# Kernel tuning notes

Measured on AMD Instinct MI355X. Metric: run time of the kernel, lower is better.

## Reference

```python
import jax, jax.numpy as jnp
import numpy as np

B, S, EMBED_DIM, FFN_DIM, N_QUBITS = 8, 4096, 768, 3072, 8

# Quantum math: each qubit starts in |0>, gets RX(x_i) then RY(theta_i), then <Z_i>.
# Since all gates are single-qubit, qubits are independent; a short derivation gives
#   <Z_i> = cos(x_i) * cos(theta_i)
# (RX(phi)|0> = (cos(phi/2), -i sin(phi/2)); apply RY(theta); |a|^2-|b|^2 = cos(theta)cos(phi)).

def setup_inputs() -> dict:
    key = jax.random.key(0)
    k1, k2, k3, k4 = jax.random.split(key, 4)
    x = jax.random.normal(k1, (B, S, EMBED_DIM), dtype=jnp.float32)
    theta = jax.random.normal(k2, (N_QUBITS,), dtype=jnp.float32)  # trainable RY angles
    W1 = jax.random.normal(k3, (FFN_DIM, N_QUBITS), dtype=jnp.float32) / np.sqrt(N_QUBITS)
    W2 = jax.random.normal(k4, (EMBED_DIM, FFN_DIM), dtype=jnp.float32) / np.sqrt(FFN_DIM)
    return {"x": x, "theta": theta, "W1": W1, "W2": W2}


def reference(x, theta, W1, W2):
    # RX-encode first N_QUBITS features of each token, RY params, PauliZ expectation.
    # Closed form of the product-state circuit: z[b,s,q] = cos(x[b,s,q]) * cos(theta[q])
    z = jnp.cos(x[..., :N_QUBITS]) * jnp.cos(theta)            # [B, S, Q]
    # dropout is identity in eval mode
    h = jax.nn.relu(jnp.einsum("bsq,fq->bsf", z, W1))          # [B, S, F]
    out = jnp.einsum("bsf,ef->bse", h, W2)                     # [B, S, E]
    return out
```

## Files before the change

kernel.cpp:

```cpp
#include <hip/hip_runtime.h>
#include <hip/hip_bf16.h>
#include <math.h>

#define T_TOK   32768
#define EDIM    768
#define FDIM    3072
#define NQ      8

#define NET     24
#define NKF     192
#define NFT     96
#define NTT     1024

#define BMQ     128
#define BNQ     192
#define NPAN    4
#define NMB     256

#define W2P_BYTES (NKF * NET * 64 * 8 * 2)
#define W1P_BYTES (NFT * 64 * 8 * 2)
#define ZP_BYTES  (NTT * 64 * 8 * 2)
#define W1P_OFFU  (W2P_BYTES / 2)
#define ZP_OFFU   ((W2P_BYTES + W1P_BYTES) / 2)
#define WS_NEED   ((size_t)(W2P_BYTES + W1P_BYTES + ZP_BYTES))

typedef float f32x16 __attribute__((ext_vector_type(16)));
typedef float f32x4  __attribute__((ext_vector_type(4)));
typedef short bf16x8 __attribute__((ext_vector_type(8)));

union FragU { uint4 u; bf16x8 v; };

static __device__ __forceinline__ unsigned pack2(float lo, float hi) {
    unsigned r;
    asm("v_cvt_pk_bf16_f32 %0, %1, %2" : "=v"(r) : "v"(lo), "v"(hi));
    return r;
}

static __device__ __forceinline__ unsigned short f2bf(float f) {
    unsigned int u = __float_as_uint(f);
    unsigned int r = (u + 0x7FFFu + ((u >> 16) & 1u)) >> 16;
    return (unsigned short)r;
}

__global__ __launch_bounds__(256) void ffq_pack(
    const float* __restrict__ x, const float* __restrict__ theta,
    const float* __restrict__ W1, const float* __restrict__ W2,
    unsigned short* __restrict__ ws)
{
    const int bid = blockIdx.x;
    unsigned short* W2P = ws;
    unsigned short* W1P = ws + W1P_OFFU;
    unsigned short* ZP  = ws + ZP_OFFU;

    if (bid < 1152) {
        const int t = bid * 256 + threadIdx.x;
        const int lane = t & 63, fe = t >> 6;
        const int kf = fe / NET, et = fe - kf * NET;
        const int g = lane >> 5, c = lane & 31;
        const int e  = et * 32 + c;
        const int f0 = kf * 16 + g * 4;
        const float4 a = *(const float4*)(W2 + (size_t)e * FDIM + f0);
        const float4 b = *(const float4*)(W2 + (size_t)e * FDIM + f0 + 8);
        FragU u;
        u.u.x = pack2(a.x, a.y); u.u.y = pack2(a.z, a.w);
        u.u.z = pack2(b.x, b.y); u.u.w = pack2(b.z, b.w);
        *(uint4*)(W2P + (((size_t)et * NKF + kf) * 64 + lane) * 8) = u.u;
    } else if (bid < 1176) {
        const int t = (bid - 1152) * 256 + threadIdx.x;
        const int lane = t & 63, ft = t >> 6;
        const int g = lane >> 5, c = lane & 31;
        FragU u; u.u = (uint4){0, 0, 0, 0};
        if (g == 0) {
            const float4 a = *(const float4*)(W1 + (size_t)(ft * 32 + c) * NQ);
            const float4 b = *(const float4*)(W1 + (size_t)(ft * 32 + c) * NQ + 4);
            u.u.x = pack2(a.x, a.y); u.u.y = pack2(a.z, a.w);
            u.u.z = pack2(b.x, b.y); u.u.w = pack2(b.z, b.w);
        }
        *(uint4*)(W1P + (size_t)t * 8) = u.u;
    } else {
        const int t = (bid - 1176) * 256 + threadIdx.x;
        const int lane = t & 63, tt = t >> 6;
        const int g = lane >> 5, c = lane & 31;
        FragU u; u.u = (uint4){0, 0, 0, 0};
        if (g == 0) {
            const int token = tt * 32 + c;
            const float4 a = *(const float4*)(x + (size_t)token * EDIM);
            const float4 b = *(const float4*)(x + (size_t)token * EDIM + 4);
            const float z0 = __cosf(a.x) * __cosf(theta[0]);
            const float z1 = __cosf(a.y) * __cosf(theta[1]);
            const float z2 = __cosf(a.z) * __cosf(theta[2]);
            const float z3 = __cosf(a.w) * __cosf(theta[3]);
            const float z4 = __cosf(b.x) * __cosf(theta[4]);
            const float z5 = __cosf(b.y) * __cosf(theta[5]);
            const float z6 = __cosf(b.z) * __cosf(theta[6]);
            const float z7 = __cosf(b.w) * __cosf(theta[7]);
            u.u.x = pack2(z0, z1); u.u.y = pack2(z2, z3);
            u.u.z = pack2(z4, z5); u.u.w = pack2(z6, z7);
        }
        *(uint4*)(ZP + (size_t)t * 8) = u.u;
    }
}

__global__ __launch_bounds__(256, 2) void ffq_main(
    const unsigned short* __restrict__ ws, float* __restrict__ out)
{
    const unsigned short* W2P = ws;
    const unsigned short* W1P = ws + W1P_OFFU;
    const unsigned short* ZP  = ws + ZP_OFFU;

    const int tid  = threadIdx.x;
    const int wave = tid >> 6;
    const int lane = tid & 63;
    const int g    = lane >> 5;
    const int c    = lane & 31;
    const int wm   = wave >> 1;
    const int wn   = wave & 1;

    const int sw    = (blockIdx.x & 7) * 128 + (blockIdx.x >> 3);
    const int panel = sw >> 8;
    const int mblk  = sw & 255;

    const int tt0 = mblk * 4 + wm * 2;
    const int et0 = panel * 6 + wn * 3;
    const size_t lo8 = (size_t)lane * 8;

    const bf16x8 zb0 = *(const bf16x8*)(ZP + (size_t)tt0 * 512 + lo8);
    const bf16x8 zb1 = *(const bf16x8*)(ZP + (size_t)(tt0 + 1) * 512 + lo8);

    const unsigned short* pB0 = W2P + (size_t)(et0 + 0) * NKF * 512 + lo8;
    const unsigned short* pB1 = W2P + (size_t)(et0 + 1) * NKF * 512 + lo8;
    const unsigned short* pB2 = W2P + (size_t)(et0 + 2) * NKF * 512 + lo8;
    const unsigned short* pW  = W1P + lo8;

    const f32x16 Zc = (f32x16)(0.f);
    f32x16 a00 = Zc, a01 = Zc, a02 = Zc, a10 = Zc, a11 = Zc, a12 = Zc;
    f32x16 d0, d1;
    bf16x8 a0l, a0h, a1l, a1h;
    bf16x8 blA0, blA1, blA2, bhA0, bhA1, bhA2;
    bf16x8 blB0, blB1, blB2, bhB0, bhB1, bhB2;
    bf16x8 wa_a, wa_b;

#define MFMA32(A, B, C) __builtin_amdgcn_mfma_f32_32x32x16_bf16((A), (B), (C), 0, 0, 0)

#define MKAF(d, o) ({                                                    \
        FragU u_;                                                        \
        u_.u.x = pack2(fmaxf((d)[(o)+0], 0.f), fmaxf((d)[(o)+1], 0.f));  \
        u_.u.y = pack2(fmaxf((d)[(o)+2], 0.f), fmaxf((d)[(o)+3], 0.f));  \
        u_.u.z = pack2(fmaxf((d)[(o)+4], 0.f), fmaxf((d)[(o)+5], 0.f));  \
        u_.u.w = pack2(fmaxf((d)[(o)+6], 0.f), fmaxf((d)[(o)+7], 0.f));  \
        u_.v; })

#define CVT() do { a0l = MKAF(d0, 0); a0h = MKAF(d0, 8);                 \
                   a1l = MKAF(d1, 0); a1h = MKAF(d1, 8); } while (0)

#define MAINLO(B0, B1, B2) do {                                          \
        a00 = MFMA32(a0l, (B0), a00); a01 = MFMA32(a0l, (B1), a01);      \
        a02 = MFMA32(a0l, (B2), a02); a10 = MFMA32(a1l, (B0), a10);      \
        a11 = MFMA32(a1l, (B1), a11); a12 = MFMA32(a1l, (B2), a12); } while (0)

#define MAINHI(B0, B1, B2) do {                                          \
        a00 = MFMA32(a0h, (B0), a00); a01 = MFMA32(a0h, (B1), a01);      \
        a02 = MFMA32(a0h, (B2), a02); a10 = MFMA32(a1h, (B0), a10);      \
        a11 = MFMA32(a1h, (B1), a11); a12 = MFMA32(a1h, (B2), a12); } while (0)

#define BODY(WALOAD, WAEXP, BL0, BL1, BL2, BH0, BH1, BH2, QLO, QHI, QW) do {   \
        WALOAD = *(const bf16x8*)(qW + (QW));                                  \
        d0 = MFMA32(WAEXP, zb0, Zc);                                           \
        d1 = MFMA32(WAEXP, zb1, Zc);                                           \
        __builtin_amdgcn_s_setprio(1);                                         \
        MAINLO(BL0, BL1, BL2);                                                 \
        __builtin_amdgcn_s_setprio(0);                                         \
        BL0 = *(const bf16x8*)(qB0 + (QLO));                                   \
        BL1 = *(const bf16x8*)(qB1 + (QLO));                                   \
        BL2 = *(const bf16x8*)(qB2 + (QLO));                                   \
        __builtin_amdgcn_s_setprio(1);                                         \
        MAINHI(BH0, BH1, BH2);                                                 \
        __builtin_amdgcn_s_setprio(0);                                         \
        BH0 = *(const bf16x8*)(qB0 + (QHI));                                   \
        BH1 = *(const bf16x8*)(qB1 + (QHI));                                   \
        BH2 = *(const bf16x8*)(qB2 + (QHI));                                   \
        CVT();                                                                 \
    } while (0)

    blA0 = *(const bf16x8*)(pB0);           blA1 = *(const bf16x8*)(pB1);
    blA2 = *(const bf16x8*)(pB2);
    bhA0 = *(const bf16x8*)(pB0 + 512);     bhA1 = *(const bf16x8*)(pB1 + 512);
    bhA2 = *(const bf16x8*)(pB2 + 512);
    blB0 = *(const bf16x8*)(pB0 + 1024);    blB1 = *(const bf16x8*)(pB1 + 1024);
    blB2 = *(const bf16x8*)(pB2 + 1024);
    bhB0 = *(const bf16x8*)(pB0 + 1536);    bhB1 = *(const bf16x8*)(pB1 + 1536);
    bhB2 = *(const bf16x8*)(pB2 + 1536);
    {
        const bf16x8 wa0 = *(const bf16x8*)(pW);
        wa_b = *(const bf16x8*)(pW + 512);
        d0 = MFMA32(wa0, zb0, Zc);
        d1 = MFMA32(wa0, zb1, Zc);
        CVT();
    }

    const unsigned short* qB0 = pB0 + 2048;
    const unsigned short* qB1 = pB1 + 2048;
    const unsigned short* qB2 = pB2 + 2048;
    const unsigned short* qW  = pW + 1024;

    #pragma unroll 1
    for (int ft = 0; ft < NFT - 2; ft += 2) {
        BODY(wa_a, wa_b, blA0, blA1, blA2, bhA0, bhA1, bhA2, 0, 512, 0);
        BODY(wa_b, wa_a, blB0, blB1, blB2, bhB0, bhB1, bhB2, 1024, 1536, 512);
        qB0 += 2048; qB1 += 2048; qB2 += 2048; qW += 1024;
    }

    d0 = MFMA32(wa_b, zb0, Zc);
    d1 = MFMA32(wa_b, zb1, Zc);
    MAINLO(blA0, blA1, blA2);
    MAINHI(bhA0, bhA1, bhA2);
    CVT();
    MAINLO(blB0, blB1, blB2);
    MAINHI(bhB0, bhB1, bhB2);

#define STORE_ACC(ACC, T, E) do {                                              \
        const size_t rb = (size_t)((tt0 + (T)) * 32 + 4 * g) * EDIM            \
                          + (size_t)(et0 + (E)) * 32 + c;                      \
        _Pragma("unroll")                                                      \
        for (int r = 0; r < 16; ++r)                                           \
            out[rb + (size_t)((r & 3) + 8 * (r >> 2)) * EDIM] = ACC[r];        \
    } while (0)

    STORE_ACC(a00, 0, 0); STORE_ACC(a01, 0, 1); STORE_ACC(a02, 0, 2);
    STORE_ACC(a10, 1, 0); STORE_ACC(a11, 1, 1); STORE_ACC(a12, 1, 2);

#undef MFMA32
#undef MKAF
#undef CVT
#undef MAINLO
#undef MAINHI
#undef BODY
#undef STORE_ACC
}

#define BM      128
#define NPANEL  6
#define NMBLK   256
#define BK      64
#define NKSTEP  (FDIM / BK)
#define HA_ST   72
#define BT_ST   72

__global__ __launch_bounds__(256) void ffq_fused(
    const float* __restrict__ x, const float* __restrict__ theta,
    const float* __restrict__ W1, const float* __restrict__ W2,
    float* __restrict__ out)
{
    __shared__ __align__(16) unsigned short hA[BM * HA_ST];
    __shared__ __align__(16) unsigned short Bt[BM * BT_ST];

    const int tid  = threadIdx.x;
    const int wave = tid >> 6;
    const int lane = tid & 63;
    const int l15  = lane & 15;
    const int lhi  = lane >> 4;
    const int wm   = wave >> 1;
    const int wn   = wave & 1;

    const int panel = blockIdx.x / NMBLK;
    const int mblk  = blockIdx.x % NMBLK;
    const int t0 = mblk * BM;
    const int n0 = panel * BM;

    bf16x8 zf[2];
    #pragma unroll
    for (int s = 0; s < 2; ++s) {
        bf16x8 z = {0, 0, 0, 0, 0, 0, 0, 0};
        if (lhi == 0) {
            const int tok = t0 + (wave * 2 + s) * 16 + l15;
            const float4* xp = (const float4*)(x + (size_t)tok * EDIM);
            const float4 x0 = xp[0];
            const float4 x1 = xp[1];
            z[0] = (short)f2bf(cosf(x0.x) * cosf(theta[0]));
            z[1] = (short)f2bf(cosf(x0.y) * cosf(theta[1]));
            z[2] = (short)f2bf(cosf(x0.z) * cosf(theta[2]));
            z[3] = (short)f2bf(cosf(x0.w) * cosf(theta[3]));
            z[4] = (short)f2bf(cosf(x1.x) * cosf(theta[4]));
            z[5] = (short)f2bf(cosf(x1.y) * cosf(theta[5]));
            z[6] = (short)f2bf(cosf(x1.z) * cosf(theta[6]));
            z[7] = (short)f2bf(cosf(x1.w) * cosf(theta[7]));
        }
        zf[s] = z;
    }

    f32x4 acc[4][4];
    #pragma unroll
    for (int mi = 0; mi < 4; ++mi)
        #pragma unroll
        for (int ni = 0; ni < 4; ++ni)
            acc[mi][ni] = (f32x4){0.f, 0.f, 0.f, 0.f};

    for (int ks = 0; ks < NKSTEP; ++ks) {
        const int k0 = ks * BK;
        __syncthreads();
        {
            const int e    = tid >> 1;
            const int half = (tid & 1) * 32;
            const float* src = W2 + (size_t)(n0 + e) * FDIM + k0 + half;
            unsigned short* dst = &Bt[e * BT_ST + half];
            #pragma unroll
            for (int i = 0; i < 4; ++i) {
                const float4 a = ((const float4*)src)[2 * i];
                const float4 b = ((const float4*)src)[2 * i + 1];
                bf16x8 v;
                v[0] = (short)f2bf(a.x); v[1] = (short)f2bf(a.y);
                v[2] = (short)f2bf(a.z); v[3] = (short)f2bf(a.w);
                v[4] = (short)f2bf(b.x); v[5] = (short)f2bf(b.y);
                v[6] = (short)f2bf(b.z); v[7] = (short)f2bf(b.w);
                *(bf16x8*)(dst + i * 8) = v;
            }
        }
        #pragma unroll
        for (int ns = 0; ns < 4; ++ns) {
            bf16x8 wf = {0, 0, 0, 0, 0, 0, 0, 0};
            if (lhi == 0) {
                const float* wp = W1 + (size_t)(k0 + ns * 16 + l15) * NQ;
                const float4 a = ((const float4*)wp)[0];
                const float4 b = ((const float4*)wp)[1];
                wf[0] = (short)f2bf(a.x); wf[1] = (short)f2bf(a.y);
                wf[2] = (short)f2bf(a.z); wf[3] = (short)f2bf(a.w);
                wf[4] = (short)f2bf(b.x); wf[5] = (short)f2bf(b.y);
                wf[6] = (short)f2bf(b.z); wf[7] = (short)f2bf(b.w);
            }
            #pragma unroll
            for (int s = 0; s < 2; ++s) {
                f32x4 hd = __builtin_amdgcn_mfma_f32_16x16x32_bf16(
                    zf[s], wf, (f32x4){0.f, 0.f, 0.f, 0.f}, 0, 0, 0);
                const int row = (wave * 2 + s) * 16 + lhi * 4;
                const int col = ns * 16 + l15;
                #pragma unroll
                for (int j = 0; j < 4; ++j) {
                    const float v = hd[j] > 0.f ? hd[j] : 0.f;
                    hA[(row + j) * HA_ST + col] = f2bf(v);
                }
            }
        }
        __syncthreads();
        #pragma unroll
        for (int ksub = 0; ksub < 2; ++ksub) {
            bf16x8 af[4], bg[4];
            #pragma unroll
            for (int mi = 0; mi < 4; ++mi) {
                const int row = wm * 64 + mi * 16 + l15;
                af[mi] = *(const bf16x8*)&hA[row * HA_ST + ksub * 32 + lhi * 8];
            }
            #pragma unroll
            for (int ni = 0; ni < 4; ++ni) {
                const int e = wn * 64 + ni * 16 + l15;
                bg[ni] = *(const bf16x8*)&Bt[e * BT_ST + ksub * 32 + lhi * 8];
            }
            #pragma unroll
            for (int mi = 0; mi < 4; ++mi)
                #pragma unroll
                for (int ni = 0; ni < 4; ++ni)
                    acc[mi][ni] = __builtin_amdgcn_mfma_f32_16x16x32_bf16(
                        af[mi], bg[ni], acc[mi][ni], 0, 0, 0);
        }
    }

    #pragma unroll
    for (int mi = 0; mi < 4; ++mi) {
        const int rbase = t0 + wm * 64 + mi * 16 + lhi * 4;
        #pragma unroll
        for (int ni = 0; ni < 4; ++ni) {
            const int cc = n0 + wn * 64 + ni * 16 + l15;
            #pragma unroll
            for (int j = 0; j < 4; ++j)
                out[(size_t)(rbase + j) * EDIM + cc] = acc[mi][ni][j];
        }
    }
}

extern "C" void kernel_launch(void* const* d_in, const int* in_sizes, int n_in,
                              void* d_out, int out_size, void* d_ws, size_t ws_size,
                              hipStream_t stream) {
    const float* x     = (const float*)d_in[0];
    const float* theta = (const float*)d_in[1];
    const float* W1    = (const float*)d_in[2];
    const float* W2    = (const float*)d_in[3];
    float* out = (float*)d_out;

    if (ws_size >= WS_NEED) {
        ffq_pack<<<dim3(1432), dim3(256), 0, stream>>>(x, theta, W1, W2,
                                                       (unsigned short*)d_ws);
        ffq_main<<<dim3(NPAN * NMB), dim3(256), 0, stream>>>(
            (const unsigned short*)d_ws, out);
    } else {
        ffq_fused<<<dim3(NPANEL * NMBLK), dim3(256), 0, stream>>>(x, theta, W1, W2, out);
    }
}
```

Baseline: 169.4 us.

## Retile ffq_main to 4 E-tiles per wave with sched_group_barrier interleaving

Changes the block-to-tile mapping so each wave computes 2 token tiles by 4 embed tiles (8 accumulators) instead of 2x3. All four waves of a block now share the same 128-column W2 panel across 256 tokens. The explicit double-buffered loop body is replaced with a single-step loop. Loads and MFMAs are interleaved using sched_group_barrier instead of setprio. The aim is more W2 fragment reuse per load and better MFMA/VMEM overlap, at the cost of more accumulator registers and possible occupancy pressure. It also reads W1 one step past the end on the last iterations (n+2), and the loop's B loads run past the K range.

```diff
diff --git a/kernel.cpp b/kernel.cpp
--- a/kernel.cpp
+++ b/kernel.cpp
@@ -12,10 +12,8 @@
 #define NFT     96
 #define NTT     1024
 
-#define BMQ     128
-#define BNQ     192
-#define NPAN    4
-#define NMB     256
+#define NMB     128
+#define NPAN    6
 
 #define W2P_BYTES (NKF * NET * 64 * 8 * 2)
 #define W1P_BYTES (NFT * 64 * 8 * 2)
@@ -101,44 +99,45 @@
     }
 }
 
+#define SGB(mask, n) __builtin_amdgcn_sched_group_barrier((mask), (n), 0)
+
 __global__ __launch_bounds__(256, 2) void ffq_main(
     const unsigned short* __restrict__ ws, float* __restrict__ out)
 {
-    const unsigned short* W2P = ws;
-    const unsigned short* W1P = ws + W1P_OFFU;
-    const unsigned short* ZP  = ws + ZP_OFFU;
+    const unsigned short* W1Pp = ws + W1P_OFFU;
+    const unsigned short* ZP   = ws + ZP_OFFU;
 
     const int tid  = threadIdx.x;
     const int wave = tid >> 6;
     const int lane = tid & 63;
     const int g    = lane >> 5;
     const int c    = lane & 31;
-    const int wm   = wave >> 1;
-    const int wn   = wave & 1;
-
-    const int sw    = (blockIdx.x & 7) * 128 + (blockIdx.x >> 3);
-    const int panel = sw >> 8;
-    const int mblk  = sw & 255;
-
-    const int tt0 = mblk * 4 + wm * 2;
-    const int et0 = panel * 6 + wn * 3;
+
+    const int sw    = (blockIdx.x & 7) * 96 + (blockIdx.x >> 3);
+    const int panel = sw / NMB;
+    const int mblk  = sw % NMB;
+
+    const int tt0 = mblk * 8 + wave * 2;
+    const int et0 = panel * 4;
     const size_t lo8 = (size_t)lane * 8;
 
     const bf16x8 zb0 = *(const bf16x8*)(ZP + (size_t)tt0 * 512 + lo8);
     const bf16x8 zb1 = *(const bf16x8*)(ZP + (size_t)(tt0 + 1) * 512 + lo8);
 
-    const unsigned short* pB0 = W2P + (size_t)(et0 + 0) * NKF * 512 + lo8;
-    const unsigned short* pB1 = W2P + (size_t)(et0 + 1) * NKF * 512 + lo8;
-    const unsigned short* pB2 = W2P + (size_t)(et0 + 2) * NKF * 512 + lo8;
-    const unsigned short* pW  = W1P + lo8;
+    const unsigned lane16 = (unsigned)lane * 16u;
+    const unsigned vo0 = (unsigned)((et0 + 0) * NKF) * 1024u + lane16;
+    const unsigned vo1 = (unsigned)((et0 + 1) * NKF) * 1024u + lane16;
+    const unsigned vo2 = (unsigned)((et0 + 2) * NKF) * 1024u + lane16;
+    const unsigned vo3 = (unsigned)((et0 + 3) * NKF) * 1024u + lane16;
+    const char* Wb = (const char*)ws;
 
     const f32x16 Zc = (f32x16)(0.f);
-    f32x16 a00 = Zc, a01 = Zc, a02 = Zc, a10 = Zc, a11 = Zc, a12 = Zc;
+    f32x16 A00 = Zc, A01 = Zc, A02 = Zc, A03 = Zc;
+    f32x16 A10 = Zc, A11 = Zc, A12 = Zc, A13 = Zc;
     f32x16 d0, d1;
     bf16x8 a0l, a0h, a1l, a1h;
-    bf16x8 blA0, blA1, blA2, bhA0, bhA1, bhA2;
-    bf16x8 blB0, blB1, blB2, bhB0, bhB1, bhB2;
-    bf16x8 wa_a, wa_b;
+    bf16x8 Bl0, Bl1, Bl2, Bl3, Bh0, Bh1, Bh2, Bh3;
+    bf16x8 wa;
 
 #define MFMA32(A, B, C) __builtin_amdgcn_mfma_f32_32x32x16_bf16((A), (B), (C), 0, 0, 0)
 
@@ -150,73 +149,56 @@
         u_.u.w = pack2(fmaxf((d)[(o)+6], 0.f), fmaxf((d)[(o)+7], 0.f));  \
         u_.v; })
 
-#define CVT() do { a0l = MKAF(d0, 0); a0h = MKAF(d0, 8);                 \
-                   a1l = MKAF(d1, 0); a1h = MKAF(d1, 8); } while (0)
-
-#define MAINLO(B0, B1, B2) do {                                          \
-        a00 = MFMA32(a0l, (B0), a00); a01 = MFMA32(a0l, (B1), a01);      \
-        a02 = MFMA32(a0l, (B2), a02); a10 = MFMA32(a1l, (B0), a10);      \
-        a11 = MFMA32(a1l, (B1), a11); a12 = MFMA32(a1l, (B2), a12); } while (0)
-
-#define MAINHI(B0, B1, B2) do {                                          \
-        a00 = MFMA32(a0h, (B0), a00); a01 = MFMA32(a0h, (B1), a01);      \
-        a02 = MFMA32(a0h, (B2), a02); a10 = MFMA32(a1h, (B0), a10);      \
-        a11 = MFMA32(a1h, (B1), a11); a12 = MFMA32(a1h, (B2), a12); } while (0)
-
-#define BODY(WALOAD, WAEXP, BL0, BL1, BL2, BH0, BH1, BH2, QLO, QHI, QW) do {   \
-        WALOAD = *(const bf16x8*)(qW + (QW));                                  \
-        d0 = MFMA32(WAEXP, zb0, Zc);                                           \
-        d1 = MFMA32(WAEXP, zb1, Zc);                                           \
-        __builtin_amdgcn_s_setprio(1);                                         \
-        MAINLO(BL0, BL1, BL2);                                                 \
-        __builtin_amdgcn_s_setprio(0);                                         \
-        BL0 = *(const bf16x8*)(qB0 + (QLO));                                   \
-        BL1 = *(const bf16x8*)(qB1 + (QLO));                                   \
-        BL2 = *(const bf16x8*)(qB2 + (QLO));                                   \
-        __builtin_amdgcn_s_setprio(1);                                         \
-        MAINHI(BH0, BH1, BH2);                                                 \
-        __builtin_amdgcn_s_setprio(0);                                         \
-        BH0 = *(const bf16x8*)(qB0 + (QHI));                                   \
-        BH1 = *(const bf16x8*)(qB1 + (QHI));                                   \
-        BH2 = *(const bf16x8*)(qB2 + (QHI));                                   \
-        CVT();                                                                 \
-    } while (0)
-
-    blA0 = *(const bf16x8*)(pB0);           blA1 = *(const bf16x8*)(pB1);
-    blA2 = *(const bf16x8*)(pB2);
-    bhA0 = *(const bf16x8*)(pB0 + 512);     bhA1 = *(const bf16x8*)(pB1 + 512);
-    bhA2 = *(const bf16x8*)(pB2 + 512);
-    blB0 = *(const bf16x8*)(pB0 + 1024);    blB1 = *(const bf16x8*)(pB1 + 1024);
-    blB2 = *(const bf16x8*)(pB2 + 1024);
-    bhB0 = *(const bf16x8*)(pB0 + 1536);    bhB1 = *(const bf16x8*)(pB1 + 1536);
-    bhB2 = *(const bf16x8*)(pB2 + 1536);
-    {
-        const bf16x8 wa0 = *(const bf16x8*)(pW);
-        wa_b = *(const bf16x8*)(pW + 512);
-        d0 = MFMA32(wa0, zb0, Zc);
-        d1 = MFMA32(wa0, zb1, Zc);
-        CVT();
-    }
-
-    const unsigned short* qB0 = pB0 + 2048;
-    const unsigned short* qB1 = pB1 + 2048;
-    const unsigned short* qB2 = pB2 + 2048;
-    const unsigned short* qW  = pW + 1024;
+    Bl0 = *(const bf16x8*)(Wb + vo0);        Bh0 = *(const bf16x8*)(Wb + vo0 + 1024);
+    Bl1 = *(const bf16x8*)(Wb + vo1);        Bh1 = *(const bf16x8*)(Wb + vo1 + 1024);
+    Bl2 = *(const bf16x8*)(Wb + vo2);        Bh2 = *(const bf16x8*)(Wb + vo2 + 1024);
+    Bl3 = *(const bf16x8*)(Wb + vo3);        Bh3 = *(const bf16x8*)(Wb + vo3 + 1024);
+    wa  = *(const bf16x8*)(W1Pp + lo8);
+    d0 = MFMA32(wa, zb0, Zc);
+    d1 = MFMA32(wa, zb1, Zc);
+    wa  = *(const bf16x8*)(W1Pp + 512 + lo8);
+    a0l = MKAF(d0, 0); a0h = MKAF(d0, 8);
+    a1l = MKAF(d1, 0); a1h = MKAF(d1, 8);
 
     #pragma unroll 1
-    for (int ft = 0; ft < NFT - 2; ft += 2) {
-        BODY(wa_a, wa_b, blA0, blA1, blA2, bhA0, bhA1, bhA2, 0, 512, 0);
-        BODY(wa_b, wa_a, blB0, blB1, blB2, bhB0, bhB1, bhB2, 1024, 1536, 512);
-        qB0 += 2048; qB1 += 2048; qB2 += 2048; qW += 1024;
-    }
-
-    d0 = MFMA32(wa_b, zb0, Zc);
-    d1 = MFMA32(wa_b, zb1, Zc);
-    MAINLO(blA0, blA1, blA2);
-    MAINHI(bhA0, bhA1, bhA2);
-    CVT();
-    MAINLO(blB0, blB1, blB2);
-    MAINHI(bhB0, bhB1, bhB2);
+    for (int n = 0; n < NFT; ++n) {
+        d0 = MFMA32(wa, zb0, Zc);
+        d1 = MFMA32(wa, zb1, Zc);
+        wa = *(const bf16x8*)(W1Pp + (size_t)(n + 2) * 512 + lo8);
+
+        A00 = MFMA32(a0l, Bl0, A00); A01 = MFMA32(a0l, Bl1, A01);
+        A02 = MFMA32(a0l, Bl2, A02); A03 = MFMA32(a0l, Bl3, A03);
+        A10 = MFMA32(a1l, Bl0, A10); A11 = MFMA32(a1l, Bl1, A11);
+        A12 = MFMA32(a1l, Bl2, A12); A13 = MFMA32(a1l, Bl3, A13);
+        Bl0 = *(const bf16x8*)(Wb + vo0 + 2048);
+        Bl1 = *(const bf16x8*)(Wb + vo1 + 2048);
+        Bl2 = *(const bf16x8*)(Wb + vo2 + 2048);
+        Bl3 = *(const bf16x8*)(Wb + vo3 + 2048);
+        a0l = MKAF(d0, 0);
+        a1l = MKAF(d1, 0);
+        SGB(0x8, 2);
+        SGB(0x8, 2); SGB(0x2, 6);
+        SGB(0x8, 2); SGB(0x2, 6);
+        SGB(0x8, 2); SGB(0x2, 6);
+        SGB(0x8, 2); SGB(0x2, 6);
+
+        A00 = MFMA32(a0h, Bh0, A00); A01 = MFMA32(a0h, Bh1, A01);
+        A02 = MFMA32(a0h, Bh2, A02); A03 = MFMA32(a0h, Bh3, A03);
+        A10 = MFMA32(a1h, Bh0, A10); A11 = MFMA32(a1h, Bh1, A11);
+        A12 = MFMA32(a1h, Bh2, A12); A13 = MFMA32(a1h, Bh3, A13);
+        Bh0 = *(const bf16x8*)(Wb + vo0 + 3072);
+        Bh1 = *(const bf16x8*)(Wb + vo1 + 3072);
+        Bh2 = *(const bf16x8*)(Wb + vo2 + 3072);
+        Bh3 = *(const bf16x8*)(Wb + vo3 + 3072);
+        a0h = MKAF(d0, 8);
+        a1h = MKAF(d1, 8);
+        SGB(0x8, 2); SGB(0x2, 6);
+        SGB(0x8, 2); SGB(0x2, 6);
+        SGB(0x8, 2); SGB(0x2, 6);
+        SGB(0x8, 2); SGB(0x2, 6);
+
+        Wb += 2048;
+    }
 
 #define STORE_ACC(ACC, T, E) do {                                              \
         const size_t rb = (size_t)((tt0 + (T)) * 32 + 4 * g) * EDIM            \
@@ -226,15 +208,11 @@
             out[rb + (size_t)((r & 3) + 8 * (r >> 2)) * EDIM] = ACC[r];        \
     } while (0)
 
-    STORE_ACC(a00, 0, 0); STORE_ACC(a01, 0, 1); STORE_ACC(a02, 0, 2);
-    STORE_ACC(a10, 1, 0); STORE_ACC(a11, 1, 1); STORE_ACC(a12, 1, 2);
+    STORE_ACC(A00, 0, 0); STORE_ACC(A01, 0, 1); STORE_ACC(A02, 0, 2); STORE_ACC(A03, 0, 3);
+    STORE_ACC(A10, 1, 0); STORE_ACC(A11, 1, 1); STORE_ACC(A12, 1, 2); STORE_ACC(A13, 1, 3);
 
 #undef MFMA32
 #undef MKAF
-#undef CVT
-#undef MAINLO
-#undef MAINHI
-#undef BODY
 #undef STORE_ACC
 }
 
```

New measurement: 152.3 us. 1.11x faster.
